# Kernel optimization log

Measured on AMD Instinct MI355X. Metric: run time of the kernel, lower is better.

## Reference

```python
import jax, jax.numpy as jnp
import numpy as np

V, D, H, B, T = 32000, 256, 512, 32, 64


def setup_inputs() -> dict:
    key = jax.random.key(0)
    ks = jax.random.split(key, 8)
    return {
        "word_indices": jax.random.randint(ks[0], (B, T), 0, V),
        "num_words": jax.random.randint(ks[1], (B,), 1, T + 1),
        "encoder_state": jax.random.normal(ks[2], (B, H), jnp.float32),
        # learned params
        "embW": jax.random.uniform(ks[3], (V, D), jnp.float32, -1.0, 1.0),
        "Wg": jax.random.normal(ks[4], (D + H, 2 * H), jnp.float32) * 0.05,  # reset+update gates
        "bg": jnp.ones((2 * H,), jnp.float32),  # TF GRUCell gate bias init = 1.0
        "Wc": jax.random.normal(ks[5], (D + H, H), jnp.float32) * 0.05,      # candidate
        "bc": jnp.zeros((H,), jnp.float32),
        "Wout": jax.random.normal(ks[6], (H, V), jnp.float32) * 0.05,        # Dense(V)
        "bout": jnp.zeros((V,), jnp.float32),
    }


def reference(word_indices, num_words, encoder_state, embW, Wg, bg, Wc, bc, Wout, bout):
    # Embedding lookup: [B, T, D] -> time-major [T, B, D]
    xs = jnp.swapaxes(embW[word_indices], 0, 1)
    # sequence-length mask like tf.nn.static_rnn: [T, B, 1]
    mask = (jnp.arange(T)[:, None] < num_words[None, :])[..., None].astype(xs.dtype)

    def step(h, inp):
        x_t, m_t = inp  # [B, D], [B, 1]
        xh = jnp.concatenate([x_t, h], axis=-1)          # [B, D+H]
        r, u = jnp.split(jax.nn.sigmoid(xh @ Wg + bg), 2, axis=-1)
        c = jnp.tanh(jnp.concatenate([x_t, r * h], axis=-1) @ Wc + bc)
        h_new = u * h + (1.0 - u) * c
        out = h_new * m_t                                 # zero outputs past seq length
        h_next = m_t * h_new + (1.0 - m_t) * h            # carry state past seq length
        return h_next, out

    _, outs = jax.lax.scan(step, encoder_state, (xs, mask))  # outs: [T, B, H]
    logits = jnp.einsum('tbh,hv->btv', outs, Wout) + bout    # [B, T, V]
    return logits
```

## Files before the change

### kernel.cpp

```cpp
#include <hip/hip_runtime.h>
#include <hip/hip_bf16.h>

#define V_ 32000
#define D_ 256
#define H_ 512
#define B_ 32
#define T_ 64
#define NSL 8

typedef __attribute__((ext_vector_type(8))) __bf16 bf16x8;
typedef __attribute__((ext_vector_type(4))) float f32x4;
typedef _Float16 f16x2 __attribute__((ext_vector_type(2)));
typedef unsigned int u32t;
typedef unsigned long long u64t;

__device__ __forceinline__ u32t pack_h16(float a, float b) {
  union { _Float16 h; unsigned short u; } lo, hi;
  lo.h = (_Float16)a; hi.h = (_Float16)b;
  return (u32t)lo.u | ((u32t)hi.u << 16);
}

__device__ __forceinline__ float dot2(u32t w, u32t h, float acc) {
#if __has_builtin(__builtin_amdgcn_fdot2)
  return __builtin_amdgcn_fdot2(__builtin_bit_cast(f16x2, w),
                                __builtin_bit_cast(f16x2, h), acc, false);
#else
  f16x2 a = __builtin_bit_cast(f16x2, w);
  f16x2 b = __builtin_bit_cast(f16x2, h);
  return acc + (float)a.x * (float)b.x + (float)a.y * (float)b.y;
#endif
}

__device__ __forceinline__ void gld_lds16(const void* g, void* l) {
  __builtin_amdgcn_global_load_lds((const __attribute__((address_space(1))) void*)g,
                                   (__attribute__((address_space(3))) void*)l,
                                   16, 0, 0);
}

__global__ __launch_bounds__(256) void k_transpose(const float* __restrict__ Wout,
                                                   __hip_bfloat16* __restrict__ WoutT) {
  __shared__ float tile[64][65];
  int v0 = blockIdx.x * 64;
  int h0 = blockIdx.y * 64;
  int tid = threadIdx.x;
#pragma unroll
  for (int i = 0; i < 16; ++i) {
    int idx = i * 256 + tid;
    int r = idx >> 6;
    int c = idx & 63;
    tile[r][c] = Wout[(size_t)(h0 + r) * V_ + v0 + c];
  }
  __syncthreads();
#pragma unroll
  for (int i = 0; i < 16; ++i) {
    int idx = i * 256 + tid;
    int rv = idx >> 6;
    int ch = idx & 63;
    WoutT[(size_t)(v0 + rv) * H_ + h0 + ch] = __float2bfloat16(tile[ch][rv]);
  }
}

__global__ __launch_bounds__(256) void k_pack_g2(const float* __restrict__ Wg,
                                                 uint4* __restrict__ Wg2) {
  int gid = blockIdx.x * 256 + threadIdx.x;
  int ks = gid & 3;
  int cq = (gid >> 2) & 127;
  int it = (gid >> 9) & 15;
  int s = gid >> 13;
  int j = (cq < 64) ? (s * 64 + cq) : (512 + s * 64 + (cq - 64));
  int k0 = ks * 128 + it * 8;
  uint4 v;
  v.x = pack_h16(Wg[(size_t)(256 + k0 + 0) * 1024 + j], Wg[(size_t)(256 + k0 + 1) * 1024 + j]);
  v.y = pack_h16(Wg[(size_t)(256 + k0 + 2) * 1024 + j], Wg[(size_t)(256 + k0 + 3) * 1024 + j]);
  v.z = pack_h16(Wg[(size_t)(256 + k0 + 4) * 1024 + j], Wg[(size_t)(256 + k0 + 5) * 1024 + j]);
  v.w = pack_h16(Wg[(size_t)(256 + k0 + 6) * 1024 + j], Wg[(size_t)(256 + k0 + 7) * 1024 + j]);
  Wg2[gid] = v;
}
__global__ __launch_bounds__(256) void k_pack_c2(const float* __restrict__ Wc,
                                                 uint4* __restrict__ Wc2) {
  int gid = blockIdx.x * 256 + threadIdx.x;
  int ks8 = gid & 7;
  int cq2 = (gid >> 3) & 63;
  int it = (gid >> 9) & 7;
  int s = gid >> 12;
  int jc = s * 64 + cq2;
  int k0 = ks8 * 64 + it * 8;
  uint4 v;
  v.x = pack_h16(Wc[(size_t)(256 + k0 + 0) * 512 + jc], Wc[(size_t)(256 + k0 + 1) * 512 + jc]);
  v.y = pack_h16(Wc[(size_t)(256 + k0 + 2) * 512 + jc], Wc[(size_t)(256 + k0 + 3) * 512 + jc]);
  v.z = pack_h16(Wc[(size_t)(256 + k0 + 4) * 512 + jc], Wc[(size_t)(256 + k0 + 5) * 512 + jc]);
  v.w = pack_h16(Wc[(size_t)(256 + k0 + 6) * 512 + jc], Wc[(size_t)(256 + k0 + 7) * 512 + jc]);
  Wc2[gid] = v;
}

__global__ __launch_bounds__(256) void k_precompute_g(const int* __restrict__ widx,
                                                      const float* __restrict__ embW,
                                                      const float* __restrict__ Wg,
                                                      const float* __restrict__ bg,
                                                      float* __restrict__ pre_g) {
  __shared__ __align__(16) float x2[D_][8];
  __shared__ int wid[8];
  int tid = threadIdx.x;
  int n0 = blockIdx.x * 8;
  if (tid < 8) wid[tid] = widx[n0 + tid];
  __syncthreads();
#pragma unroll
  for (int i = 0; i < 8; ++i)
    x2[tid][i] = embW[(size_t)wid[i] * D_ + tid];
  __syncthreads();

  int J = blockIdx.y * 256 + tid;
  float bias = bg[J];
  float acc[8];
#pragma unroll
  for (int i = 0; i < 8; ++i) acc[i] = bias;
  for (int d = 0; d < D_; ++d) {
    float4 xa = *(const float4*)&x2[d][0];
    float4 xb = *(const float4*)&x2[d][4];
    float w = Wg[(size_t)d * 1024 + J];
    acc[0] = fmaf(xa.x, w, acc[0]); acc[1] = fmaf(xa.y, w, acc[1]);
    acc[2] = fmaf(xa.z, w, acc[2]); acc[3] = fmaf(xa.w, w, acc[3]);
    acc[4] = fmaf(xb.x, w, acc[4]); acc[5] = fmaf(xb.y, w, acc[5]);
    acc[6] = fmaf(xb.z, w, acc[6]); acc[7] = fmaf(xb.w, w, acc[7]);
  }
#pragma unroll
  for (int i = 0; i < 8; ++i)
    pre_g[(size_t)(n0 + i) * 1024 + J] = acc[i];
}

__global__ __launch_bounds__(256) void k_precompute_c(const int* __restrict__ widx,
                                                      const float* __restrict__ embW,
                                                      const float* __restrict__ Wc,
                                                      const float* __restrict__ bc,
                                                      float* __restrict__ pre_c) {
  __shared__ __align__(16) float x2[D_][8];
  __shared__ int wid[8];
  int tid = threadIdx.x;
  int n0 = blockIdx.x * 8;
  if (tid < 8) wid[tid] = widx[n0 + tid];
  __syncthreads();
#pragma unroll
  for (int i = 0; i < 8; ++i)
    x2[tid][i] = embW[(size_t)wid[i] * D_ + tid];
  __syncthreads();

  int Jc = blockIdx.y * 256 + tid;
  float bias = bc[Jc];
  float acc[8];
#pragma unroll
  for (int i = 0; i < 8; ++i) acc[i] = bias;
  for (int d = 0; d < D_; ++d) {
    float4 xa = *(const float4*)&x2[d][0];
    float4 xb = *(const float4*)&x2[d][4];
    float w = Wc[(size_t)d * 512 + Jc];
    acc[0] = fmaf(xa.x, w, acc[0]); acc[1] = fmaf(xa.y, w, acc[1]);
    acc[2] = fmaf(xa.z, w, acc[2]); acc[3] = fmaf(xa.w, w, acc[3]);
    acc[4] = fmaf(xb.x, w, acc[4]); acc[5] = fmaf(xb.y, w, acc[5]);
    acc[6] = fmaf(xb.z, w, acc[6]); acc[7] = fmaf(xb.w, w, acc[7]);
  }
#pragma unroll
  for (int i = 0; i < 8; ++i)
    pre_c[(size_t)(n0 + i) * 512 + Jc] = acc[i];
}

__global__ __launch_bounds__(256) void k_gru_init(const float* __restrict__ enc,
                                                  u32t* __restrict__ HB,
                                                  int* __restrict__ flags) {
  int gid = blockIdx.x * 256 + threadIdx.x;
  int b = gid >> 8, wk = gid & 255;
  u32t v = pack_h16(enc[b * H_ + 2 * wk], enc[b * H_ + 2 * wk + 1]);
  __hip_atomic_store(&HB[gid], v, __ATOMIC_RELAXED, __HIP_MEMORY_SCOPE_AGENT);
#pragma unroll
  for (int i = 0; i < 4; ++i)
    __hip_atomic_store(&flags[gid * 4 + i], 0, __ATOMIC_RELAXED, __HIP_MEMORY_SCOPE_AGENT);
}

__global__ __launch_bounds__(512, 2) void k_gru5(const int* __restrict__ num_words,
                                                 const uint4* __restrict__ Wg2,
                                                 const uint4* __restrict__ Wc2,
                                                 const float* __restrict__ pre_g,
                                                 const float* __restrict__ pre_c,
                                                 u32t* __restrict__ RH,
                                                 u32t* __restrict__ HB,
                                                 int* __restrict__ flagR,
                                                 int* __restrict__ flagH,
                                                 u32t* __restrict__ A32) {
  __shared__ __align__(16) u32t h2_l[256];
  __shared__ __align__(16) u32t rh2_l[256];
  __shared__ float u_l[64];
  int bid = blockIdx.x;
  int b = bid & 31;
  int s = bid >> 5;
  int tid = threadIdx.x;
  int nw = num_words[b];

  int cq = tid >> 2, ks = tid & 3;
  int j1 = (cq < 64) ? (s * 64 + cq) : (512 + s * 64 + (cq - 64));
  int cq2 = tid >> 3, ks8 = tid & 7;
  int jc = s * 64 + cq2;

  uint4 wg[16];
#pragma unroll
  for (int i = 0; i < 16; ++i) {
    int ii = (i + ks) & 15;
    wg[i] = Wg2[(((size_t)s * 16 + ii) * 128 + cq) * 4 + ks];
  }
  uint4 wc[8];
#pragma unroll
  for (int i = 0; i < 8; ++i) {
    int ii = (i + ks8) & 7;
    wc[i] = Wc2[(((size_t)s * 8 + ii) * 64 + cq2) * 8 + ks8];
  }

  const u64t* HB64 = (const u64t*)HB;
  const u64t* RH64 = (const u64t*)RH;
  int* fR = flagR + b * 512;
  int* fH = flagH + b * 512;

  for (int t = 0; t < T_; ++t) {
    float pg = pre_g[((size_t)b * T_ + t) * 1024 + j1];
    float pc = pre_c[((size_t)b * T_ + t) * 512 + jc];

    if (tid < 64) {
      u64t v = __hip_atomic_load(&HB64[(size_t)b * 128 + 2 * tid], __ATOMIC_RELAXED,
                                 __HIP_MEMORY_SCOPE_AGENT);
      u64t v2 = __hip_atomic_load(&HB64[(size_t)b * 128 + 2 * tid + 1], __ATOMIC_RELAXED,
                                  __HIP_MEMORY_SCOPE_AGENT);
      *(u64t*)&h2_l[4 * tid] = v;
      *(u64t*)&h2_l[4 * tid + 2] = v2;
    }
    __syncthreads();

    float a = 0.f;
    const uint4* h4 = (const uint4*)h2_l;
#pragma unroll
    for (int i = 0; i < 16; ++i) {
      int ii = (i + ks) & 15;
      uint4 hv = h4[ks * 16 + ii];
      a = dot2(wg[i].x, hv.x, a);
      a = dot2(wg[i].y, hv.y, a);
      a = dot2(wg[i].z, hv.z, a);
      a = dot2(wg[i].w, hv.w, a);
    }
    a += __shfl_xor(a, 1);
    a += __shfl_xor(a, 2);
    float gate = 1.f / (1.f + __expf(-(a + pg)));
    if (cq < 64) {
      u32t hw = h2_l[(s * 64 + cq) >> 1];
      f16x2 hp = __builtin_bit_cast(f16x2, hw);
      float hh = (cq & 1) ? (float)hp.y : (float)hp.x;
      u32t mine = pack_h16(gate * hh, 0.f) & 0xffffu;
      u32t oth = (u32t)__shfl_xor((int)mine, 4);
      if (ks == 0 && (cq & 1) == 0)
        __hip_atomic_store(&RH[(size_t)b * 256 + s * 32 + (cq >> 1)],
                           mine | (oth << 16), __ATOMIC_RELAXED,
                           __HIP_MEMORY_SCOPE_AGENT);
    } else if (ks == 0) {
      u_l[cq - 64] = gate;
    }

    asm volatile("s_waitcnt vmcnt(0)" ::: "memory");
    __syncthreads();
    if (tid == 0)
      __hip_atomic_store(&fR[s * 64], t + 1, __ATOMIC_RELAXED, __HIP_MEMORY_SCOPE_AGENT);
    if (tid < NSL) {
      while (__hip_atomic_load(&fR[tid * 64], __ATOMIC_RELAXED, __HIP_MEMORY_SCOPE_AGENT) < t + 1)
        __builtin_amdgcn_s_sleep(1);
    }
    __syncthreads();

    if (tid < 64) {
      u64t v = __hip_atomic_load(&RH64[(size_t)b * 128 + 2 * tid], __ATOMIC_RELAXED,
                                 __HIP_MEMORY_SCOPE_AGENT);
      u64t v2 = __hip_atomic_load(&RH64[(size_t)b * 128 + 2 * tid + 1], __ATOMIC_RELAXED,
                                  __HIP_MEMORY_SCOPE_AGENT);
      *(u64t*)&rh2_l[4 * tid] = v;
      *(u64t*)&rh2_l[4 * tid + 2] = v2;
    }
    __syncthreads();

    float a2 = 0.f;
    const uint4* r4 = (const uint4*)rh2_l;
#pragma unroll
    for (int i = 0; i < 8; ++i) {
      int ii = (i + ks8) & 7;
      uint4 rv = r4[ks8 * 8 + ii];
      a2 = dot2(wc[i].x, rv.x, a2);
      a2 = dot2(wc[i].y, rv.y, a2);
      a2 = dot2(wc[i].z, rv.z, a2);
      a2 = dot2(wc[i].w, rv.w, a2);
    }
    a2 += __shfl_xor(a2, 1);
    a2 += __shfl_xor(a2, 2);
    a2 += __shfl_xor(a2, 4);
    float cv = tanhf(a2 + pc);
    float uu = u_l[cq2];
    u32t hw = h2_l[jc >> 1];
    f16x2 hp = __builtin_bit_cast(f16x2, hw);
    float hold = (cq2 & 1) ? (float)hp.y : (float)hp.x;
    float hn = uu * hold + (1.f - uu) * cv;
    bool live = t < nw;
    float hnext = live ? hn : hold;
    u32t mh = pack_h16(hnext, 0.f) & 0xffffu;
    u32t ma = (u32t)__hip_bfloat16_raw(__float2bfloat16(live ? hn : 0.f)).x;
    u32t oh = (u32t)__shfl_xor((int)mh, 8);
    u32t oa = (u32t)__shfl_xor((int)ma, 8);
    bool writer = (ks8 == 0) && ((cq2 & 1) == 0);
    if (writer)
      __hip_atomic_store(&HB[(size_t)b * 256 + s * 32 + (cq2 >> 1)],
                         mh | (oh << 16), __ATOMIC_RELAXED, __HIP_MEMORY_SCOPE_AGENT);

    asm volatile("s_waitcnt vmcnt(0)" ::: "memory");
    __syncthreads();
    if (tid == 0)
      __hip_atomic_store(&fH[s * 64], t + 1, __ATOMIC_RELAXED, __HIP_MEMORY_SCOPE_AGENT);
    if (writer)
      A32[(((size_t)b * T_ + t) * 512 + jc) >> 1] = ma | (oa << 16);
    if (tid < NSL) {
      while (__hip_atomic_load(&fH[tid * 64], __ATOMIC_RELAXED, __HIP_MEMORY_SCOPE_AGENT) < t + 1)
        __builtin_amdgcn_s_sleep(1);
    }
    __syncthreads();
  }
}

__global__ __launch_bounds__(256) void k_proj(const __hip_bfloat16* __restrict__ Ap,
                                              const __hip_bfloat16* __restrict__ BTp,
                                              const float* __restrict__ bout,
                                              float* __restrict__ C) {
  __shared__ char As[128 * 64 * 2];
  __shared__ char Bs[128 * 64 * 2];
  int tid = threadIdx.x;
  int lane = tid & 63;
  int wave = tid >> 6;
  int m0 = blockIdx.x * 128;
  int n0 = blockIdx.y * 128;
  int wm = wave >> 1, wn = wave & 1;
  f32x4 acc[4][4] = {};

  const char* Ab = (const char*)Ap;
  const char* Bb = (const char*)BTp;

  for (int ks = 0; ks < 8; ++ks) {
    int k0 = ks * 64;
    __syncthreads();
#pragma unroll
    for (int inst = 0; inst < 4; ++inst) {
      int o = inst * 4096 + wave * 1024;
      int ol = o + lane * 16;
      int r = ol >> 7;
      int cb = ol & 127;
      gld_lds16(Ab + ((size_t)(m0 + r) * 512 + k0) * 2 + cb, As + o);
      gld_lds16(Bb + ((size_t)(n0 + r) * 512 + k0) * 2 + cb, Bs + o);
    }
    __syncthreads();
#pragma unroll
    for (int kk = 0; kk < 64; kk += 32) {
      bf16x8 af[4], bfr[4];
      int cbyte = kk * 2 + ((lane >> 4) << 4);
#pragma unroll
      for (int mi = 0; mi < 4; ++mi) {
        int row = wm * 64 + mi * 16 + (lane & 15);
        af[mi] = *(const bf16x8*)(As + row * 128 + cbyte);
      }
#pragma unroll
      for (int ni = 0; ni < 4; ++ni) {
        int row = wn * 64 + ni * 16 + (lane & 15);
        bfr[ni] = *(const bf16x8*)(Bs + row * 128 + cbyte);
      }
#pragma unroll
      for (int mi = 0; mi < 4; ++mi)
#pragma unroll
        for (int ni = 0; ni < 4; ++ni)
          acc[mi][ni] = __builtin_amdgcn_mfma_f32_16x16x32_bf16(af[mi], bfr[ni], acc[mi][ni], 0, 0, 0);
    }
  }
#pragma unroll
  for (int ni = 0; ni < 4; ++ni) {
    int col = n0 + wn * 64 + ni * 16 + (lane & 15);
    float bb = bout[col];
#pragma unroll
    for (int mi = 0; mi < 4; ++mi) {
      int rbase = m0 + wm * 64 + mi * 16 + ((lane >> 4) << 2);
#pragma unroll
      for (int rr = 0; rr < 4; ++rr) {
        C[(size_t)(rbase + rr) * V_ + col] = acc[mi][ni][rr] + bb;
      }
    }
  }
}

extern "C" void kernel_launch(void* const* d_in, const int* in_sizes, int n_in,
                              void* d_out, int out_size, void* d_ws, size_t ws_size,
                              hipStream_t stream) {
  const int* widx = (const int*)d_in[0];
  const int* num_words = (const int*)d_in[1];
  const float* enc = (const float*)d_in[2];
  const float* embW = (const float*)d_in[3];
  const float* Wg = (const float*)d_in[4];
  const float* bg = (const float*)d_in[5];
  const float* Wc = (const float*)d_in[6];
  const float* bc = (const float*)d_in[7];
  const float* Wout = (const float*)d_in[8];
  const float* bout = (const float*)d_in[9];
  float* out = (float*)d_out;

  char* ws = (char*)d_ws;
  float* pre_g = (float*)(ws);
  float* pre_c = (float*)(ws + 8388608);
  __hip_bfloat16* A = (__hip_bfloat16*)(ws + 12582912);
  __hip_bfloat16* WoutT = (__hip_bfloat16*)(ws + 14680064);
  uint4* Wg2 = (uint4*)(ws + 47448064);
  uint4* Wc2 = (uint4*)(ws + 48496640);
  u32t* RH = (u32t*)(ws + 49020928);
  u32t* HB = (u32t*)(ws + 49053696);
  int* flags = (int*)(ws + 49086464);
  int* flagR = flags;
  int* flagH = flags + 16384;

  hipLaunchKernelGGL(k_pack_g2, dim3(256), dim3(256), 0, stream, Wg, Wg2);
  hipLaunchKernelGGL(k_pack_c2, dim3(128), dim3(256), 0, stream, Wc, Wc2);
  hipLaunchKernelGGL(k_transpose, dim3(500, 8), dim3(256), 0, stream, Wout, WoutT);
  hipLaunchKernelGGL(k_precompute_g, dim3(256, 4), dim3(256), 0, stream,
                     widx, embW, Wg, bg, pre_g);
  hipLaunchKernelGGL(k_precompute_c, dim3(256, 2), dim3(256), 0, stream,
                     widx, embW, Wc, bc, pre_c);
  hipLaunchKernelGGL(k_gru_init, dim3(32), dim3(256), 0, stream, enc, HB, flags);
  hipLaunchKernelGGL(k_gru5, dim3(32 * NSL), dim3(512), 0, stream,
                     num_words, Wg2, Wc2, pre_g, pre_c, RH, HB, flagR, flagH, (u32t*)A);
  hipLaunchKernelGGL(k_proj, dim3(16, 250), dim3(256), 0, stream, A, WoutT, bout, out);
}
```

Baseline: 446.8 us.

## Batch four sequences per GRU block and move wait to start of step

The recurrent GRU kernel now has each block handle four batch rows for one hidden slice, so the grid shrinks from 256 blocks to 64. Register-resident weights are reused across four sequences and the per-step flag traffic is shared. The wait on the new hidden state moves from the end of a step to the start of the next one, which lets the A output writes overlap with other blocks. In exchange each block does four times the serial dot-product work per step, and fewer CUs are occupied.

```diff
diff --git a/kernel.cpp b/kernel.cpp
--- a/kernel.cpp
+++ b/kernel.cpp
@@ -7,6 +7,7 @@
 #define B_ 32
 #define T_ 64
 #define NSL 8
+#define NB 4
 
 typedef __attribute__((ext_vector_type(8))) __bf16 bf16x8;
 typedef __attribute__((ext_vector_type(4))) float f32x4;
@@ -35,6 +36,16 @@
   __builtin_amdgcn_global_load_lds((const __attribute__((address_space(1))) void*)g,
                                    (__attribute__((address_space(3))) void*)l,
                                    16, 0, 0);
+}
+
+__device__ __forceinline__ u32t ld_rlx(const u32t* p) {
+  return __hip_atomic_load(p, __ATOMIC_RELAXED, __HIP_MEMORY_SCOPE_AGENT);
+}
+__device__ __forceinline__ u64t ld_rlx64(const u64t* p) {
+  return __hip_atomic_load(p, __ATOMIC_RELAXED, __HIP_MEMORY_SCOPE_AGENT);
+}
+__device__ __forceinline__ void st_rlx(u32t* p, u32t v) {
+  __hip_atomic_store(p, v, __ATOMIC_RELAXED, __HIP_MEMORY_SCOPE_AGENT);
 }
 
 __global__ __launch_bounds__(256) void k_transpose(const float* __restrict__ Wout,
@@ -169,13 +180,13 @@
   int gid = blockIdx.x * 256 + threadIdx.x;
   int b = gid >> 8, wk = gid & 255;
   u32t v = pack_h16(enc[b * H_ + 2 * wk], enc[b * H_ + 2 * wk + 1]);
-  __hip_atomic_store(&HB[gid], v, __ATOMIC_RELAXED, __HIP_MEMORY_SCOPE_AGENT);
+  st_rlx(&HB[gid], v);
 #pragma unroll
   for (int i = 0; i < 4; ++i)
-    __hip_atomic_store(&flags[gid * 4 + i], 0, __ATOMIC_RELAXED, __HIP_MEMORY_SCOPE_AGENT);
-}
-
-__global__ __launch_bounds__(512, 2) void k_gru5(const int* __restrict__ num_words,
+    st_rlx((u32t*)&flags[gid * 4 + i], 0);
+}
+
+__global__ __launch_bounds__(512, 2) void k_gru6(const int* __restrict__ num_words,
                                                  const uint4* __restrict__ Wg2,
                                                  const uint4* __restrict__ Wc2,
                                                  const float* __restrict__ pre_g,
@@ -185,14 +196,13 @@
                                                  int* __restrict__ flagR,
                                                  int* __restrict__ flagH,
                                                  u32t* __restrict__ A32) {
-  __shared__ __align__(16) u32t h2_l[256];
-  __shared__ __align__(16) u32t rh2_l[256];
-  __shared__ float u_l[64];
+  __shared__ __align__(16) u32t h2_l[NB][256];
+  __shared__ __align__(16) u32t rh2_l[NB][256];
+  __shared__ float u_l[NB][64];
   int bid = blockIdx.x;
-  int b = bid & 31;
-  int s = bid >> 5;
+  int s = bid >> 3;
+  int g = bid & 7;
   int tid = threadIdx.x;
-  int nw = num_words[b];
 
   int cq = tid >> 2, ks = tid & 3;
   int j1 = (cq < 64) ? (s * 64 + cq) : (512 + s * 64 + (cq - 64));
@@ -212,115 +222,135 @@
     wc[i] = Wc2[(((size_t)s * 8 + ii) * 64 + cq2) * 8 + ks8];
   }
 
+  int nw[NB];
+#pragma unroll
+  for (int q = 0; q < NB; ++q) nw[q] = num_words[4 * g + q];
+
   const u64t* HB64 = (const u64t*)HB;
   const u64t* RH64 = (const u64t*)RH;
-  int* fR = flagR + b * 512;
-  int* fH = flagH + b * 512;
+  int pb = 4 * g + (tid >> 3);
+  int pflag_off = pb * 512 + (tid & 7) * 64;
+
+  int sq = tid >> 6, sl = tid & 63;
+  int sb = 4 * g + sq;
+
+  bool writer1 = (ks == 0) && ((cq & 1) == 0) && (cq < 64);
+  bool ulane = (ks == 0) && (cq >= 64);
+  bool writer2 = (ks8 == 0) && ((cq2 & 1) == 0);
 
   for (int t = 0; t < T_; ++t) {
-    float pg = pre_g[((size_t)b * T_ + t) * 1024 + j1];
-    float pc = pre_c[((size_t)b * T_ + t) * 512 + jc];
-
-    if (tid < 64) {
-      u64t v = __hip_atomic_load(&HB64[(size_t)b * 128 + 2 * tid], __ATOMIC_RELAXED,
-                                 __HIP_MEMORY_SCOPE_AGENT);
-      u64t v2 = __hip_atomic_load(&HB64[(size_t)b * 128 + 2 * tid + 1], __ATOMIC_RELAXED,
-                                  __HIP_MEMORY_SCOPE_AGENT);
-      *(u64t*)&h2_l[4 * tid] = v;
-      *(u64t*)&h2_l[4 * tid + 2] = v2;
-    }
-    __syncthreads();
-
-    float a = 0.f;
-    const uint4* h4 = (const uint4*)h2_l;
-#pragma unroll
-    for (int i = 0; i < 16; ++i) {
-      int ii = (i + ks) & 15;
-      uint4 hv = h4[ks * 16 + ii];
-      a = dot2(wg[i].x, hv.x, a);
-      a = dot2(wg[i].y, hv.y, a);
-      a = dot2(wg[i].z, hv.z, a);
-      a = dot2(wg[i].w, hv.w, a);
-    }
-    a += __shfl_xor(a, 1);
-    a += __shfl_xor(a, 2);
-    float gate = 1.f / (1.f + __expf(-(a + pg)));
-    if (cq < 64) {
-      u32t hw = h2_l[(s * 64 + cq) >> 1];
+    float pg[NB], pc[NB];
+#pragma unroll
+    for (int q = 0; q < NB; ++q) {
+      pg[q] = pre_g[((size_t)(4 * g + q) * T_ + t) * 1024 + j1];
+      pc[q] = pre_c[((size_t)(4 * g + q) * T_ + t) * 512 + jc];
+    }
+
+    if (tid < 32) {
+      const u32t* fp = (const u32t*)&flagH[pflag_off];
+      while ((int)ld_rlx(fp) < t) __builtin_amdgcn_s_sleep(1);
+    }
+    __syncthreads();
+    if (tid < 256) {
+      u64t v = ld_rlx64(&HB64[(size_t)sb * 128 + 2 * sl]);
+      u64t v2 = ld_rlx64(&HB64[(size_t)sb * 128 + 2 * sl + 1]);
+      *(u64t*)&h2_l[sq][4 * sl] = v;
+      *(u64t*)&h2_l[sq][4 * sl + 2] = v2;
+    }
+    __syncthreads();
+
+#pragma unroll
+    for (int q = 0; q < NB; ++q) {
+      int b = 4 * g + q;
+      float a = 0.f;
+      const uint4* h4 = (const uint4*)&h2_l[q][0];
+#pragma unroll
+      for (int i = 0; i < 16; ++i) {
+        int ii = (i + ks) & 15;
+        uint4 hv = h4[ks * 16 + ii];
+        a = dot2(wg[i].x, hv.x, a);
+        a = dot2(wg[i].y, hv.y, a);
+        a = dot2(wg[i].z, hv.z, a);
+        a = dot2(wg[i].w, hv.w, a);
+      }
+      a += __shfl_xor(a, 1);
+      a += __shfl_xor(a, 2);
+      float gate = 1.f / (1.f + __expf(-(a + pg[q])));
+      if (cq < 64) {
+        u32t hw = h2_l[q][(s * 64 + cq) >> 1];
+        f16x2 hp = __builtin_bit_cast(f16x2, hw);
+        float hh = (cq & 1) ? (float)hp.y : (float)hp.x;
+        u32t mine = pack_h16(gate * hh, 0.f) & 0xffffu;
+        u32t oth = (u32t)__shfl_xor((int)mine, 4);
+        if (writer1)
+          st_rlx(&RH[(size_t)b * 256 + s * 32 + (cq >> 1)], mine | (oth << 16));
+      } else if (ulane) {
+        u_l[q][cq - 64] = gate;
+      }
+    }
+
+    asm volatile("s_waitcnt vmcnt(0)" ::: "memory");
+    __syncthreads();
+    if (tid < NB)
+      st_rlx((u32t*)&flagR[(4 * g + tid) * 512 + s * 64], (u32t)(t + 1));
+
+    if (tid < 32) {
+      const u32t* fp = (const u32t*)&flagR[pflag_off];
+      while ((int)ld_rlx(fp) < t + 1) __builtin_amdgcn_s_sleep(1);
+    }
+    __syncthreads();
+    if (tid < 256) {
+      u64t v = ld_rlx64(&RH64[(size_t)sb * 128 + 2 * sl]);
+      u64t v2 = ld_rlx64(&RH64[(size_t)sb * 128 + 2 * sl + 1]);
+      *(u64t*)&rh2_l[sq][4 * sl] = v;
+      *(u64t*)&rh2_l[sq][4 * sl + 2] = v2;
+    }
+    __syncthreads();
+
+    u32t aw[NB];
+#pragma unroll
+    for (int q = 0; q < NB; ++q) {
+      int b = 4 * g + q;
+      float a2 = 0.f;
+      const uint4* r4 = (const uint4*)&rh2_l[q][0];
+#pragma unroll
+      for (int i = 0; i < 8; ++i) {
+        int ii = (i + ks8) & 7;
+        uint4 rv = r4[ks8 * 8 + ii];
+        a2 = dot2(wc[i].x, rv.x, a2);
+        a2 = dot2(wc[i].y, rv.y, a2);
+        a2 = dot2(wc[i].z, rv.z, a2);
+        a2 = dot2(wc[i].w, rv.w, a2);
+      }
+      a2 += __shfl_xor(a2, 1);
+      a2 += __shfl_xor(a2, 2);
+      a2 += __shfl_xor(a2, 4);
+      float cv = tanhf(a2 + pc[q]);
+      float uu = u_l[q][cq2];
+      u32t hw = h2_l[q][jc >> 1];
       f16x2 hp = __builtin_bit_cast(f16x2, hw);
-      float hh = (cq & 1) ? (float)hp.y : (float)hp.x;
-      u32t mine = pack_h16(gate * hh, 0.f) & 0xffffu;
-      u32t oth = (u32t)__shfl_xor((int)mine, 4);
-      if (ks == 0 && (cq & 1) == 0)
-        __hip_atomic_store(&RH[(size_t)b * 256 + s * 32 + (cq >> 1)],
-                           mine | (oth << 16), __ATOMIC_RELAXED,
-                           __HIP_MEMORY_SCOPE_AGENT);
-    } else if (ks == 0) {
-      u_l[cq - 64] = gate;
+      float hold = (cq2 & 1) ? (float)hp.y : (float)hp.x;
+      float hn = uu * hold + (1.f - uu) * cv;
+      bool live = t < nw[q];
+      float hnext = live ? hn : hold;
+      u32t mh = pack_h16(hnext, 0.f) & 0xffffu;
+      u32t ma = (u32t)__hip_bfloat16_raw(__float2bfloat16(live ? hn : 0.f)).x;
+      u32t oh = (u32t)__shfl_xor((int)mh, 8);
+      u32t oa = (u32t)__shfl_xor((int)ma, 8);
+      aw[q] = ma | (oa << 16);
+      if (writer2)
+        st_rlx(&HB[(size_t)b * 256 + s * 32 + (cq2 >> 1)], mh | (oh << 16));
     }
 
     asm volatile("s_waitcnt vmcnt(0)" ::: "memory");
     __syncthreads();
-    if (tid == 0)
-      __hip_atomic_store(&fR[s * 64], t + 1, __ATOMIC_RELAXED, __HIP_MEMORY_SCOPE_AGENT);
-    if (tid < NSL) {
-      while (__hip_atomic_load(&fR[tid * 64], __ATOMIC_RELAXED, __HIP_MEMORY_SCOPE_AGENT) < t + 1)
-        __builtin_amdgcn_s_sleep(1);
-    }
-    __syncthreads();
-
-    if (tid < 64) {
-      u64t v = __hip_atomic_load(&RH64[(size_t)b * 128 + 2 * tid], __ATOMIC_RELAXED,
-                                 __HIP_MEMORY_SCOPE_AGENT);
-      u64t v2 = __hip_atomic_load(&RH64[(size_t)b * 128 + 2 * tid + 1], __ATOMIC_RELAXED,
-                                  __HIP_MEMORY_SCOPE_AGENT);
-      *(u64t*)&rh2_l[4 * tid] = v;
-      *(u64t*)&rh2_l[4 * tid + 2] = v2;
-    }
-    __syncthreads();
-
-    float a2 = 0.f;
-    const uint4* r4 = (const uint4*)rh2_l;
-#pragma unroll
-    for (int i = 0; i < 8; ++i) {
-      int ii = (i + ks8) & 7;
-      uint4 rv = r4[ks8 * 8 + ii];
-      a2 = dot2(wc[i].x, rv.x, a2);
-      a2 = dot2(wc[i].y, rv.y, a2);
-      a2 = dot2(wc[i].z, rv.z, a2);
-      a2 = dot2(wc[i].w, rv.w, a2);
-    }
-    a2 += __shfl_xor(a2, 1);
-    a2 += __shfl_xor(a2, 2);
-    a2 += __shfl_xor(a2, 4);
-    float cv = tanhf(a2 + pc);
-    float uu = u_l[cq2];
-    u32t hw = h2_l[jc >> 1];
-    f16x2 hp = __builtin_bit_cast(f16x2, hw);
-    float hold = (cq2 & 1) ? (float)hp.y : (float)hp.x;
-    float hn = uu * hold + (1.f - uu) * cv;
-    bool live = t < nw;
-    float hnext = live ? hn : hold;
-    u32t mh = pack_h16(hnext, 0.f) & 0xffffu;
-    u32t ma = (u32t)__hip_bfloat16_raw(__float2bfloat16(live ? hn : 0.f)).x;
-    u32t oh = (u32t)__shfl_xor((int)mh, 8);
-    u32t oa = (u32t)__shfl_xor((int)ma, 8);
-    bool writer = (ks8 == 0) && ((cq2 & 1) == 0);
-    if (writer)
-      __hip_atomic_store(&HB[(size_t)b * 256 + s * 32 + (cq2 >> 1)],
-                         mh | (oh << 16), __ATOMIC_RELAXED, __HIP_MEMORY_SCOPE_AGENT);
-
-    asm volatile("s_waitcnt vmcnt(0)" ::: "memory");
-    __syncthreads();
-    if (tid == 0)
-      __hip_atomic_store(&fH[s * 64], t + 1, __ATOMIC_RELAXED, __HIP_MEMORY_SCOPE_AGENT);
-    if (writer)
-      A32[(((size_t)b * T_ + t) * 512 + jc) >> 1] = ma | (oa << 16);
-    if (tid < NSL) {
-      while (__hip_atomic_load(&fH[tid * 64], __ATOMIC_RELAXED, __HIP_MEMORY_SCOPE_AGENT) < t + 1)
-        __builtin_amdgcn_s_sleep(1);
-    }
-    __syncthreads();
+    if (tid < NB)
+      st_rlx((u32t*)&flagH[(4 * g + tid) * 512 + s * 64], (u32t)(t + 1));
+    if (writer2) {
+#pragma unroll
+      for (int q = 0; q < NB; ++q)
+        A32[((size_t)(4 * g + q) * T_ + t) * 256 + s * 32 + (cq2 >> 1)] = aw[q];
+    }
   }
 }
 
@@ -426,7 +456,7 @@
   hipLaunchKernelGGL(k_precompute_c, dim3(256, 2), dim3(256), 0, stream,
                      widx, embW, Wc, bc, pre_c);
   hipLaunchKernelGGL(k_gru_init, dim3(32), dim3(256), 0, stream, enc, HB, flags);
-  hipLaunchKernelGGL(k_gru5, dim3(32 * NSL), dim3(512), 0, stream,
+  hipLaunchKernelGGL(k_gru6, dim3(64), dim3(512), 0, stream,
                      num_words, Wg2, Wc2, pre_g, pre_c, RH, HB, flagR, flagH, (u32t*)A);
   hipLaunchKernelGGL(k_proj, dim3(16, 250), dim3(256), 0, stream, A, WoutT, bout, out);
 }
```

After: 610.0 us. 1.37x slower.

## Replace flag-based grid barriers with step-tagged data words in GRU recurrence

Applied to the files above, without the earlier changes.

Each fp16 hidden-state and r*h element is now stored in its own 32-bit word with the step index in the upper 16 bits. Consumers spin directly on the data until the tag matches, so the separate flag store, the vmcnt wait and the extra block barriers per phase go away. The intent is to cut inter-block synchronisation latency on the sequential critical path. In exchange every thread polls global memory and buffer traffic doubles, and the scheme relies on relaxed atomics keeping value and tag consistent within a single word.

```diff
diff --git a/kernel.cpp b/kernel.cpp
--- a/kernel.cpp
+++ b/kernel.cpp
@@ -12,12 +12,19 @@
 typedef __attribute__((ext_vector_type(4))) float f32x4;
 typedef _Float16 f16x2 __attribute__((ext_vector_type(2)));
 typedef unsigned int u32t;
+typedef unsigned short u16t;
 typedef unsigned long long u64t;
 
 __device__ __forceinline__ u32t pack_h16(float a, float b) {
   union { _Float16 h; unsigned short u; } lo, hi;
   lo.h = (_Float16)a; hi.h = (_Float16)b;
   return (u32t)lo.u | ((u32t)hi.u << 16);
+}
+
+__device__ __forceinline__ float f16u_to_f(u16t u) {
+  union { _Float16 h; unsigned short u; } x;
+  x.u = u;
+  return (float)x.h;
 }
 
 __device__ __forceinline__ float dot2(u32t w, u32t h, float acc) {
@@ -35,6 +42,13 @@
   __builtin_amdgcn_global_load_lds((const __attribute__((address_space(1))) void*)g,
                                    (__attribute__((address_space(3))) void*)l,
                                    16, 0, 0);
+}
+
+__device__ __forceinline__ u32t ld_rlx(const u32t* p) {
+  return __hip_atomic_load(p, __ATOMIC_RELAXED, __HIP_MEMORY_SCOPE_AGENT);
+}
+__device__ __forceinline__ void st_rlx(u32t* p, u32t v) {
+  __hip_atomic_store(p, v, __ATOMIC_RELAXED, __HIP_MEMORY_SCOPE_AGENT);
 }
 
 __global__ __launch_bounds__(256) void k_transpose(const float* __restrict__ Wout,
@@ -164,26 +178,22 @@
 }
 
 __global__ __launch_bounds__(256) void k_gru_init(const float* __restrict__ enc,
-                                                  u32t* __restrict__ HB,
-                                                  int* __restrict__ flags) {
+                                                  u32t* __restrict__ HBT,
+                                                  u32t* __restrict__ RHT) {
   int gid = blockIdx.x * 256 + threadIdx.x;
-  int b = gid >> 8, wk = gid & 255;
-  u32t v = pack_h16(enc[b * H_ + 2 * wk], enc[b * H_ + 2 * wk + 1]);
-  __hip_atomic_store(&HB[gid], v, __ATOMIC_RELAXED, __HIP_MEMORY_SCOPE_AGENT);
-#pragma unroll
-  for (int i = 0; i < 4; ++i)
-    __hip_atomic_store(&flags[gid * 4 + i], 0, __ATOMIC_RELAXED, __HIP_MEMORY_SCOPE_AGENT);
-}
-
-__global__ __launch_bounds__(512, 2) void k_gru5(const int* __restrict__ num_words,
+  int b = gid >> 9, k = gid & 511;
+  u32t hv = pack_h16(enc[b * H_ + k], 0.f) & 0xffffu;
+  st_rlx(&HBT[gid], hv);
+  st_rlx(&RHT[gid], 0xFFFF0000u);
+}
+
+__global__ __launch_bounds__(512, 2) void k_gru7(const int* __restrict__ num_words,
                                                  const uint4* __restrict__ Wg2,
                                                  const uint4* __restrict__ Wc2,
                                                  const float* __restrict__ pre_g,
                                                  const float* __restrict__ pre_c,
-                                                 u32t* __restrict__ RH,
-                                                 u32t* __restrict__ HB,
-                                                 int* __restrict__ flagR,
-                                                 int* __restrict__ flagH,
+                                                 u32t* __restrict__ RHT,
+                                                 u32t* __restrict__ HBT,
                                                  u32t* __restrict__ A32) {
   __shared__ __align__(16) u32t h2_l[256];
   __shared__ __align__(16) u32t rh2_l[256];
@@ -212,22 +222,23 @@
     wc[i] = Wc2[(((size_t)s * 8 + ii) * 64 + cq2) * 8 + ks8];
   }
 
-  const u64t* HB64 = (const u64t*)HB;
-  const u64t* RH64 = (const u64t*)RH;
-  int* fR = flagR + b * 512;
-  int* fH = flagH + b * 512;
+  u32t* HBp = HBT + (size_t)b * 512;
+  u32t* RHp = RHT + (size_t)b * 512;
+  bool pub1 = (ks == 0) && (cq < 64);
+  bool ulane = (ks == 0) && (cq >= 64);
+  bool pub2 = (ks8 == 0);
+  bool writer2 = pub2 && ((cq2 & 1) == 0);
 
   for (int t = 0; t < T_; ++t) {
     float pg = pre_g[((size_t)b * T_ + t) * 1024 + j1];
     float pc = pre_c[((size_t)b * T_ + t) * 512 + jc];
 
-    if (tid < 64) {
-      u64t v = __hip_atomic_load(&HB64[(size_t)b * 128 + 2 * tid], __ATOMIC_RELAXED,
-                                 __HIP_MEMORY_SCOPE_AGENT);
-      u64t v2 = __hip_atomic_load(&HB64[(size_t)b * 128 + 2 * tid + 1], __ATOMIC_RELAXED,
-                                  __HIP_MEMORY_SCOPE_AGENT);
-      *(u64t*)&h2_l[4 * tid] = v;
-      *(u64t*)&h2_l[4 * tid + 2] = v2;
+    __syncthreads();
+    {
+      u32t want = (u32t)t << 16;
+      u32t v;
+      do { v = ld_rlx(&HBp[tid]); } while ((v & 0xffff0000u) != want);
+      ((volatile u16t*)h2_l)[tid] = (u16t)v;
     }
     __syncthreads();
 
@@ -246,36 +257,19 @@
     a += __shfl_xor(a, 2);
     float gate = 1.f / (1.f + __expf(-(a + pg)));
     if (cq < 64) {
-      u32t hw = h2_l[(s * 64 + cq) >> 1];
-      f16x2 hp = __builtin_bit_cast(f16x2, hw);
-      float hh = (cq & 1) ? (float)hp.y : (float)hp.x;
-      u32t mine = pack_h16(gate * hh, 0.f) & 0xffffu;
-      u32t oth = (u32t)__shfl_xor((int)mine, 4);
-      if (ks == 0 && (cq & 1) == 0)
-        __hip_atomic_store(&RH[(size_t)b * 256 + s * 32 + (cq >> 1)],
-                           mine | (oth << 16), __ATOMIC_RELAXED,
-                           __HIP_MEMORY_SCOPE_AGENT);
-    } else if (ks == 0) {
+      float hh = f16u_to_f(((const u16t*)h2_l)[s * 64 + cq]);
+      if (pub1)
+        st_rlx(&RHp[s * 64 + cq],
+               (pack_h16(gate * hh, 0.f) & 0xffffu) | ((u32t)(t + 1) << 16));
+    } else if (ulane) {
       u_l[cq - 64] = gate;
     }
 
-    asm volatile("s_waitcnt vmcnt(0)" ::: "memory");
-    __syncthreads();
-    if (tid == 0)
-      __hip_atomic_store(&fR[s * 64], t + 1, __ATOMIC_RELAXED, __HIP_MEMORY_SCOPE_AGENT);
-    if (tid < NSL) {
-      while (__hip_atomic_load(&fR[tid * 64], __ATOMIC_RELAXED, __HIP_MEMORY_SCOPE_AGENT) < t + 1)
-        __builtin_amdgcn_s_sleep(1);
-    }
-    __syncthreads();
-
-    if (tid < 64) {
-      u64t v = __hip_atomic_load(&RH64[(size_t)b * 128 + 2 * tid], __ATOMIC_RELAXED,
-                                 __HIP_MEMORY_SCOPE_AGENT);
-      u64t v2 = __hip_atomic_load(&RH64[(size_t)b * 128 + 2 * tid + 1], __ATOMIC_RELAXED,
-                                  __HIP_MEMORY_SCOPE_AGENT);
-      *(u64t*)&rh2_l[4 * tid] = v;
-      *(u64t*)&rh2_l[4 * tid + 2] = v2;
+    {
+      u32t want = (u32t)(t + 1) << 16;
+      u32t v;
+      do { v = ld_rlx(&RHp[tid]); } while ((v & 0xffff0000u) != want);
+      ((volatile u16t*)rh2_l)[tid] = (u16t)v;
     }
     __syncthreads();
 
@@ -295,32 +289,17 @@
     a2 += __shfl_xor(a2, 4);
     float cv = tanhf(a2 + pc);
     float uu = u_l[cq2];
-    u32t hw = h2_l[jc >> 1];
-    f16x2 hp = __builtin_bit_cast(f16x2, hw);
-    float hold = (cq2 & 1) ? (float)hp.y : (float)hp.x;
+    float hold = f16u_to_f(((const u16t*)h2_l)[jc]);
     float hn = uu * hold + (1.f - uu) * cv;
     bool live = t < nw;
     float hnext = live ? hn : hold;
-    u32t mh = pack_h16(hnext, 0.f) & 0xffffu;
+    if (pub2)
+      st_rlx(&HBp[s * 64 + cq2],
+             (pack_h16(hnext, 0.f) & 0xffffu) | ((u32t)(t + 1) << 16));
     u32t ma = (u32t)__hip_bfloat16_raw(__float2bfloat16(live ? hn : 0.f)).x;
-    u32t oh = (u32t)__shfl_xor((int)mh, 8);
     u32t oa = (u32t)__shfl_xor((int)ma, 8);
-    bool writer = (ks8 == 0) && ((cq2 & 1) == 0);
-    if (writer)
-      __hip_atomic_store(&HB[(size_t)b * 256 + s * 32 + (cq2 >> 1)],
-                         mh | (oh << 16), __ATOMIC_RELAXED, __HIP_MEMORY_SCOPE_AGENT);
-
-    asm volatile("s_waitcnt vmcnt(0)" ::: "memory");
-    __syncthreads();
-    if (tid == 0)
-      __hip_atomic_store(&fH[s * 64], t + 1, __ATOMIC_RELAXED, __HIP_MEMORY_SCOPE_AGENT);
-    if (writer)
+    if (writer2)
       A32[(((size_t)b * T_ + t) * 512 + jc) >> 1] = ma | (oa << 16);
-    if (tid < NSL) {
-      while (__hip_atomic_load(&fH[tid * 64], __ATOMIC_RELAXED, __HIP_MEMORY_SCOPE_AGENT) < t + 1)
-        __builtin_amdgcn_s_sleep(1);
-    }
-    __syncthreads();
   }
 }
 
@@ -412,11 +391,8 @@
   __hip_bfloat16* WoutT = (__hip_bfloat16*)(ws + 14680064);
   uint4* Wg2 = (uint4*)(ws + 47448064);
   uint4* Wc2 = (uint4*)(ws + 48496640);
-  u32t* RH = (u32t*)(ws + 49020928);
-  u32t* HB = (u32t*)(ws + 49053696);
-  int* flags = (int*)(ws + 49086464);
-  int* flagR = flags;
-  int* flagH = flags + 16384;
+  u32t* RHT = (u32t*)(ws + 49020928);
+  u32t* HBT = (u32t*)(ws + 49086464);
 
   hipLaunchKernelGGL(k_pack_g2, dim3(256), dim3(256), 0, stream, Wg, Wg2);
   hipLaunchKernelGGL(k_pack_c2, dim3(128), dim3(256), 0, stream, Wc, Wc2);
@@ -425,8 +401,8 @@
                      widx, embW, Wg, bg, pre_g);
   hipLaunchKernelGGL(k_precompute_c, dim3(256, 2), dim3(256), 0, stream,
                      widx, embW, Wc, bc, pre_c);
-  hipLaunchKernelGGL(k_gru_init, dim3(32), dim3(256), 0, stream, enc, HB, flags);
-  hipLaunchKernelGGL(k_gru5, dim3(32 * NSL), dim3(512), 0, stream,
-                     num_words, Wg2, Wc2, pre_g, pre_c, RH, HB, flagR, flagH, (u32t*)A);
+  hipLaunchKernelGGL(k_gru_init, dim3(64), dim3(256), 0, stream, enc, HBT, RHT);
+  hipLaunchKernelGGL(k_gru7, dim3(32 * NSL), dim3(512), 0, stream,
+                     num_words, Wg2, Wc2, pre_g, pre_c, RHT, HBT, (u32t*)A);
   hipLaunchKernelGGL(k_proj, dim3(16, 250), dim3(256), 0, stream, A, WoutT, bout, out);
 }
```

After: 390.5 us. 1.14x faster.
